# Kernel tuning notes

Measured on AMD Instinct MI355X. Metric: run time of the kernel, lower is better.

The kernel has to match this reference:

```python
import jax, jax.numpy as jnp
import numpy as np

B, QT, N, E, H = 4, 1024, 2048, 512, 8
Dh = E // H
ROPE_BASE = 10000.0


def rope_cos_sin_from_pos(pos_idx, Dh, base=10000.0, dtype=jnp.float32):
    # pos_idx: [B, T] -> cos, sin: [B, T, Dh]
    half = Dh // 2
    freqs = 1.0 / base ** (jnp.arange(0, half, dtype=dtype) / half)
    ang = pos_idx.astype(dtype)[..., None] * freqs[None, None, :]
    cos = jnp.repeat(jnp.cos(ang), 2, axis=-1)
    sin = jnp.repeat(jnp.sin(ang), 2, axis=-1)
    return cos, sin


def rope_apply(x_hd, cos, sin):
    # x_hd: [B, H, T, Dh]; cos/sin: [B, 1, T, Dh] (only first Dh//2 used, as in source)
    D = x_hd.shape[-1]
    x2 = x_hd.reshape(*x_hd.shape[:-1], D // 2, 2)
    x1, xi = x2[..., 0], x2[..., 1]
    c = cos[..., :D // 2]
    s = sin[..., :D // 2]
    y1 = x1 * c - xi * s
    y2 = x1 * s + xi * c
    return jnp.stack([y1, y2], axis=-1).reshape(*x_hd.shape)


def setup_inputs() -> dict:
    key = jax.random.key(0)
    ks = jax.random.split(key, 16)
    scale_w = 1.0 / np.sqrt(E)
    inp = {
        "q": jax.random.normal(ks[0], (B, QT, E), jnp.float32),
        "kv": jax.random.normal(ks[1], (B, N, E), jnp.float32),
        "q_mask": jax.random.randint(ks[2], (B, QT), 0, 2) > 0,
        "kv_mask": jax.random.randint(ks[3], (B, N), 0, 2) > 0,
        "q_pos_idx": jnp.sort(jax.random.randint(ks[4], (B, QT), 0, 4096), axis=-1).astype(jnp.int32),
        "kv_pos_idx": jnp.sort(jax.random.randint(ks[5], (B, N), 0, 4096), axis=-1).astype(jnp.int32),
        "Wq": jax.random.normal(ks[6], (E, E), jnp.float32) * scale_w,
        "bq": jnp.zeros((E,), jnp.float32),
        "Wk": jax.random.normal(ks[7], (E, E), jnp.float32) * scale_w,
        "bk": jnp.zeros((E,), jnp.float32),
        "Wv": jax.random.normal(ks[8], (E, E), jnp.float32) * scale_w,
        "bv": jnp.zeros((E,), jnp.float32),
        "Wo": jax.random.normal(ks[9], (E, E), jnp.float32) * scale_w,
        "bo": jnp.zeros((E,), jnp.float32),
    }
    return inp


def reference(q, kv, q_mask, kv_mask, q_pos_idx, kv_pos_idx,
              Wq, bq, Wk, bk, Wv, bv, Wo, bo):
    scale = 1.0 / jnp.sqrt(jnp.array(Dh, dtype=q.dtype))
    # projections -> [B, H, T, Dh]
    qh = (q @ Wq + bq).reshape(B, QT, H, Dh).transpose(0, 2, 1, 3)
    kh = (kv @ Wk + bk).reshape(B, N, H, Dh).transpose(0, 2, 1, 3)
    vh = (kv @ Wv + bv).reshape(B, N, H, Dh).transpose(0, 2, 1, 3)
    # per-sample RoPE
    cos_q, sin_q = rope_cos_sin_from_pos(q_pos_idx, Dh, ROPE_BASE, qh.dtype)
    cos_k, sin_k = rope_cos_sin_from_pos(kv_pos_idx, Dh, ROPE_BASE, kh.dtype)
    qh = rope_apply(qh, cos_q[:, None], sin_q[:, None])
    kh = rope_apply(kh, cos_k[:, None], sin_k[:, None])
    # scores [B, H, Q, N]
    scores = jnp.einsum("bhqd,bhkd->bhqk", qh, kh) * scale
    kvm = kv_mask[:, None, None, :].astype(bool)
    scores = jnp.where(kvm, scores, jnp.full_like(scores, -1e9))
    attn = jax.nn.softmax(scores, axis=-1)
    # dropout_rate=0 / deterministic -> identity; post-softmax mask + renorm
    attn = attn * kvm
    attn = attn / (attn.sum(-1, keepdims=True) + 1e-9)
    ctx = jnp.einsum("bhqk,bhkd->bhqd", attn, vh)
    ctx = ctx.transpose(0, 2, 1, 3).reshape(B, QT, E)
    ctx = ctx @ Wo + bo
    ctx = ctx * q_mask.astype(ctx.dtype)[:, :, None]
    return ctx, attn
```

## Files before the change

kernel.cpp:

```cpp
#include <hip/hip_runtime.h>
#include <hip/hip_bf16.h>

#define B_  4
#define QT_ 1024
#define N_  2048
#define E_  512
#define H_  8
#define DH_ 64

typedef float  f32x4  __attribute__((ext_vector_type(4)));
typedef __bf16 bf16x8 __attribute__((ext_vector_type(8)));
typedef unsigned short u16;
typedef u16 u16x4 __attribute__((ext_vector_type(4)));

static __device__ __forceinline__ u16 f2bf(float f) {
    unsigned u = __builtin_bit_cast(unsigned, f);
    return (u16)((u + 0x7fffu + ((u >> 16) & 1u)) >> 16);
}

static __device__ __forceinline__ bf16x8 ldbf8(const u16* p) {
    uint4 v = *reinterpret_cast<const uint4*>(p);
    return __builtin_bit_cast(bf16x8, v);
}

#define MFMA16(a, b, c) __builtin_amdgcn_mfma_f32_16x16x32_bf16((a), (b), (c), 0, 0, 0)

static __device__ __forceinline__ void g2lds16(const u16* g, u16* l) {
    __builtin_amdgcn_global_load_lds((__attribute__((address_space(1))) void*)(void*)g,
                                     (__attribute__((address_space(3))) void*)l, 16, 0, 0);
}

__global__ __launch_bounds__(256) void cvt_all(const float* __restrict__ q,
                                               const float* __restrict__ kv,
                                               u16* __restrict__ qbf,
                                               u16* __restrict__ kvbf) {
    const int QN4 = B_ * QT_ * E_ / 4;
    int i = blockIdx.x * 256 + threadIdx.x;
    const float4* s;
    ushort4* d;
    if (i < QN4) {
        s = reinterpret_cast<const float4*>(q) + i;
        d = reinterpret_cast<ushort4*>(qbf) + i;
    } else {
        int j = i - QN4;
        s = reinterpret_cast<const float4*>(kv) + j;
        d = reinterpret_cast<ushort4*>(kvbf) + j;
    }
    float4 v = *s;
    ushort4 o;
    o.x = f2bf(v.x); o.y = f2bf(v.y); o.z = f2bf(v.z); o.w = f2bf(v.w);
    *d = o;
}

__global__ __launch_bounds__(256) void wt_all(const float* __restrict__ Wq,
                                              const float* __restrict__ Wk,
                                              const float* __restrict__ Wv,
                                              const float* __restrict__ Wo,
                                              u16* __restrict__ wt4) {
    __shared__ float t[64][65];
    const float* W = (blockIdx.z == 0) ? Wq : (blockIdx.z == 1) ? Wk : (blockIdx.z == 2) ? Wv : Wo;
    u16* dst = wt4 + (size_t)blockIdx.z * E_ * E_;
    int k0 = blockIdx.x * 64, n0 = blockIdx.y * 64;
    int tid = threadIdx.x;
#pragma unroll
    for (int i = 0; i < 16; i++) {
        int idx = tid + i * 256, r = idx >> 6, c = idx & 63;
        t[r][c] = W[(k0 + r) * E_ + n0 + c];
    }
    __syncthreads();
#pragma unroll
    for (int i = 0; i < 16; i++) {
        int idx = tid + i * 256, r = idx >> 6, c = idx & 63;
        dst[(n0 + r) * E_ + k0 + c] = f2bf(t[c][r]);
    }
}

__global__ __launch_bounds__(256) void rope_all(const int* __restrict__ qpos,
                                                const int* __restrict__ kvpos,
                                                float2* __restrict__ tq,
                                                float2* __restrict__ tk) {
    const int QROWS = B_ * QT_;
    int i = blockIdx.x * 256 + threadIdx.x;
    int k = i & 15, row = i >> 4;
    float fr = exp2f((float)k * -0.41524101186092028f);
    int p;
    float2* dst;
    if (row < QROWS) { p = qpos[row]; dst = tq + i; }
    else { p = kvpos[row - QROWS]; dst = tk + (i - QROWS * 16); }
    float sn, cs;
    sincosf((float)p * fr, &sn, &cs);
    *dst = make_float2(cs, sn);
}

__global__ __launch_bounds__(256) void proj_qkv(const u16* __restrict__ qbf,
                                                const u16* __restrict__ kvbf,
                                                const u16* __restrict__ wt4,
                                                const float* __restrict__ bq,
                                                const float* __restrict__ bk,
                                                const float* __restrict__ bv,
                                                u16* __restrict__ qhh,
                                                u16* __restrict__ khh,
                                                u16* __restrict__ vt,
                                                const float2* __restrict__ tq,
                                                const float2* __restrict__ tk) {
    __shared__ __align__(16) u16 la[2][128 * 32];
    __shared__ __align__(16) u16 lb[2][128 * 32];

    const int id = blockIdx.x;
    const int sw = (id & 7) * 80 + (id >> 3);
    const bool isQ = (sw < 128);
    int m0, n0;
    const u16 *X, *W;
    if (isQ) { m0 = (sw >> 2) * 128; n0 = (sw & 3) * 128; X = qbf; W = wt4; }
    else { const int s2 = sw - 128; m0 = (s2 >> 3) * 128; n0 = (s2 & 7) * 128; X = kvbf; W = wt4 + 512 * 512; }

    const int tid = threadIdx.x, w = tid >> 6, lane = tid & 63;
    const int lr = lane & 15, lg = lane >> 4;
    const int wml = (w >> 1) * 64, wnl = (w & 1) * 64;

    auto stage = [&](const u16* gsrc, u16* lbuf) {
#pragma unroll
        for (int i = 0; i < 2; i++) {
            const int r0 = w * 32 + i * 16;
            const int row = r0 + (lane >> 2);
            const u16* src = gsrc + row * E_ + (((lane & 3) ^ (row & 3)) * 8);
            g2lds16(src, lbuf + r0 * 32);
        }
    };

    f32x4 acc[4][4];
#pragma unroll
    for (int i = 0; i < 4; i++)
#pragma unroll
        for (int j = 0; j < 4; j++) acc[i][j] = f32x4{0.f, 0.f, 0.f, 0.f};

    stage(X + m0 * E_, la[0]);
    stage(W + n0 * E_, lb[0]);
    __syncthreads();
    int buf = 0;
    for (int kt = 0; kt < E_ / 32; kt++) {
        if (kt + 1 < E_ / 32) {
            stage(X + m0 * E_ + (kt + 1) * 32, la[buf ^ 1]);
            stage(W + n0 * E_ + (kt + 1) * 32, lb[buf ^ 1]);
        }
        bf16x8 a[4], bb[4];
#pragma unroll
        for (int mb = 0; mb < 4; mb++) {
            const int r = wml + mb * 16 + lr;
            a[mb] = ldbf8(la[buf] + r * 32 + ((lg ^ (r & 3)) * 8));
        }
#pragma unroll
        for (int nb = 0; nb < 4; nb++) {
            const int r = wnl + nb * 16 + lr;
            bb[nb] = ldbf8(lb[buf] + r * 32 + ((lg ^ (r & 3)) * 8));
        }
        __builtin_amdgcn_s_setprio(1);
#pragma unroll
        for (int mb = 0; mb < 4; mb++)
#pragma unroll
            for (int nb = 0; nb < 4; nb++)
                acc[mb][nb] = MFMA16(a[mb], bb[nb], acc[mb][nb]);
        __builtin_amdgcn_s_setprio(0);
        __syncthreads();
        buf ^= 1;
    }

    const bool isV = !isQ && (n0 >= 512);
#pragma unroll
    for (int mb = 0; mb < 4; mb++) {
#pragma unroll
        for (int nb = 0; nb < 4; nb++) {
            const int col = n0 + wnl + nb * 16 + lr;
            const float bs = isQ ? bq[col] : (isV ? bv[col - 512] : bk[col]);
#pragma unroll
            for (int r = 0; r < 4; r++) {
                const int row = m0 + wml + mb * 16 + lg * 4 + r;
                float v = acc[mb][nb][r] + bs;
                if (isV) {
                    const int cv = col - 512, d = cv & 63, h = cv >> 6;
                    const int b = row >> 11, n = row & 2047;
                    vt[(((b * H_ + h) * (N_ / 64) + (n >> 6)) * DH_ + d) * 64 + (n & 63)] = f2bf(v);
                } else {
                    const int d = col & 63, h = col >> 6;
                    float2 t = isQ ? tq[row * 16 + (d >> 2)] : tk[row * 16 + (d >> 2)];
                    float other = __shfl_xor(v, 1);
                    float y = (d & 1) ? (other * t.y + v * t.x) : (v * t.x - other * t.y);
                    if (isQ) {
                        y *= 0.125f;
                        const int b = row >> 10, tok = row & 1023;
                        qhh[((b * H_ + h) * QT_ + tok) * DH_ + d] = f2bf(y);
                    } else {
                        const int b = row >> 11, tok = row & 2047;
                        khh[((b * H_ + h) * N_ + tok) * DH_ + d] = f2bf(y);
                    }
                }
            }
        }
    }
}

__global__ __launch_bounds__(256) void attn_sums(const u16* __restrict__ qh,
                                                 const u16* __restrict__ kh,
                                                 const int* __restrict__ kv_mask,
                                                 float* __restrict__ sums4) {
    __shared__ __align__(16) u16 kbuf[2][64 * 64];

    const int id = blockIdx.x;
    const int sw = (id & 7) * 256 + (id >> 3);
    const int bh = sw >> 6, qt = (sw >> 2) & 15, ns = sw & 3;
    const int b = bh >> 3;
    const int tid = threadIdx.x, w = tid >> 6, lane = tid & 63;
    const int lr = lane & 15, lg = lane >> 4;
    const int q0 = qt * 64 + w * 16;

    const u16* qbase = qh + (bh * QT_ + q0) * DH_;
    const bf16x8 qf0 = ldbf8(qbase + lr * DH_ + lg * 8);
    const bf16x8 qf1 = ldbf8(qbase + lr * DH_ + 32 + lg * 8);
    const u16* kbase = kh + (size_t)bh * (N_ * DH_) + ns * 512 * DH_;
    const int* mbase = kv_mask + b * N_ + ns * 512;

    auto stage = [&](const u16* gsrc, u16* lbuf) {
#pragma unroll
        for (int i = 0; i < 2; i++) {
            const int r0 = w * 16 + i * 8;
            const int row = r0 + (lane >> 3);
            const u16* src = gsrc + row * 64 + (((lane & 7) ^ (row & 7)) * 8);
            g2lds16(src, lbuf + r0 * 64);
        }
    };

    float lsum[4] = {0.f, 0.f, 0.f, 0.f};
    stage(kbase, kbuf[0]);
    __syncthreads();
    for (int t = 0; t < 8; t++) {
        const u16* kc = kbuf[t & 1];
        if (t < 7) stage(kbase + (t + 1) * (64 * DH_), kbuf[(t + 1) & 1]);
#pragma unroll
        for (int n = 0; n < 4; n++) {
            const int krow = n * 16 + lr;
            const u16* kp = kc + krow * 64;
            bf16x8 k0 = ldbf8(kp + ((lg ^ (krow & 7)) * 8));
            bf16x8 k1 = ldbf8(kp + (((lg + 4) ^ (krow & 7)) * 8));
            f32x4 c = f32x4{0.f, 0.f, 0.f, 0.f};
            __builtin_amdgcn_s_setprio(1);
            c = MFMA16(qf0, k0, c);
            c = MFMA16(qf1, k1, c);
            __builtin_amdgcn_s_setprio(0);
            const bool keep = (mbase[t * 64 + n * 16 + lr] != 0);
#pragma unroll
            for (int r = 0; r < 4; r++) lsum[r] += keep ? __expf(c[r]) : 0.f;
        }
        __syncthreads();
    }
#pragma unroll
    for (int r = 0; r < 4; r++) {
        float s = lsum[r];
        s += __shfl_xor(s, 1); s += __shfl_xor(s, 2);
        s += __shfl_xor(s, 4); s += __shfl_xor(s, 8);
        if (lr == 0) sums4[((size_t)bh * QT_ + q0 + lg * 4 + r) * 4 + ns] = s;
    }
}

__global__ __launch_bounds__(256) void attn_pv(const u16* __restrict__ qh,
                                               const u16* __restrict__ kh,
                                               const u16* __restrict__ vt,
                                               const int* __restrict__ kv_mask,
                                               const float* __restrict__ sums4,
                                               float* __restrict__ attn_out,
                                               float* __restrict__ pvpart) {
    __shared__ __align__(16) u16 kbuf[2][64 * 64];
    __shared__ __align__(16) u16 vbuf[2][64 * 64];
    __shared__ unsigned PW[4][16][32];

    const int id = blockIdx.x;
    const int sw = (id & 7) * 128 + (id >> 3);
    const int bh = sw >> 5, qt = (sw >> 1) & 15, ns = sw & 1;
    const int b = bh >> 3;
    const int tid = threadIdx.x, w = tid >> 6, lane = tid & 63;
    const int lr = lane & 15, lg = lane >> 4;
    const int q0 = qt * 64 + w * 16;

    const u16* qbase = qh + (bh * QT_ + q0) * DH_;
    const bf16x8 qf0 = ldbf8(qbase + lr * DH_ + lg * 8);
    const bf16x8 qf1 = ldbf8(qbase + lr * DH_ + 32 + lg * 8);
    const u16* kbase = kh + (size_t)bh * (N_ * DH_) + ns * 1024 * DH_;
    const u16* vbase = vt + (size_t)bh * (N_ * DH_) + ns * 1024 * DH_;
    const int* mbase = kv_mask + b * N_ + ns * 1024;

    float inv[4];
#pragma unroll
    for (int r = 0; r < 4; r++) {
        float4 s4 = *reinterpret_cast<const float4*>(
            sums4 + ((size_t)bh * QT_ + q0 + lg * 4 + r) * 4);
        float tot = s4.x + s4.y + s4.z + s4.w;
        inv[r] = (tot > 0.f) ? (1.0f / tot) : 0.f;
    }

    auto stage = [&](const u16* gsrc, u16* lbuf) {
#pragma unroll
        for (int i = 0; i < 2; i++) {
            const int r0 = w * 16 + i * 8;
            const int row = r0 + (lane >> 3);
            const u16* src = gsrc + row * 64 + (((lane & 7) ^ (row & 7)) * 8);
            g2lds16(src, lbuf + r0 * 64);
        }
    };

    f32x4 pv[4];
#pragma unroll
    for (int i = 0; i < 4; i++) pv[i] = f32x4{0.f, 0.f, 0.f, 0.f};
    unsigned(*P)[32] = PW[w];
    float* abase = attn_out + ((size_t)(bh * QT_ + q0)) * N_ + ns * 1024;
    const int srow = lane >> 4, cq = lane & 15;

    stage(kbase, kbuf[0]);
    stage(vbase, vbuf[0]);
    __syncthreads();
    for (int t = 0; t < 16; t++) {
        const u16* kc = kbuf[t & 1];
        const u16* vc = vbuf[t & 1];
        if (t < 15) {
            stage(kbase + (t + 1) * (64 * DH_), kbuf[(t + 1) & 1]);
            stage(vbase + (t + 1) * (64 * DH_), vbuf[(t + 1) & 1]);
        }
#pragma unroll
        for (int n = 0; n < 4; n++) {
            const int krow = n * 16 + lr;
            const u16* kp = kc + krow * 64;
            bf16x8 k0 = ldbf8(kp + ((lg ^ (krow & 7)) * 8));
            bf16x8 k1 = ldbf8(kp + (((lg + 4) ^ (krow & 7)) * 8));
            f32x4 c = f32x4{0.f, 0.f, 0.f, 0.f};
            __builtin_amdgcn_s_setprio(1);
            c = MFMA16(qf0, k0, c);
            c = MFMA16(qf1, k1, c);
            __builtin_amdgcn_s_setprio(0);
            const bool keep = (mbase[t * 64 + n * 16 + lr] != 0);
#pragma unroll
            for (int r = 0; r < 4; r++) {
                float p = keep ? (__expf(c[r]) * inv[r]) : 0.f;
                float hi = __shfl_xor(p, 1);
                __bf16 lo_b = (__bf16)p, hi_b = (__bf16)hi;
                unsigned pk = ((unsigned)__builtin_bit_cast(u16, hi_b) << 16) |
                              (unsigned)__builtin_bit_cast(u16, lo_b);
                if (!(lr & 1)) {
                    const int row = lg * 4 + r, c32 = n * 8 + (lr >> 1);
                    P[row][(((c32 >> 2) ^ (row & 7)) << 2) + (c32 & 3)] = pk;
                }
            }
        }
#pragma unroll
        for (int i = 0; i < 4; i++) {
            const int row = i * 4 + srow, rw = row & 7;
            const int m = (((cq >> 1) ^ rw) << 2) + ((cq & 1) << 1);
            uint2 pp = *reinterpret_cast<const uint2*>(&P[row][m]);
            f32x4 vv;
            vv[0] = __builtin_bit_cast(float, pp.x << 16);
            vv[1] = __builtin_bit_cast(float, pp.x & 0xffff0000u);
            vv[2] = __builtin_bit_cast(float, pp.y << 16);
            vv[3] = __builtin_bit_cast(float, pp.y & 0xffff0000u);
            *reinterpret_cast<f32x4*>(abase + (size_t)row * N_ + t * 64 + cq * 4) = vv;
        }
#pragma unroll
        for (int ks = 0; ks < 2; ks++) {
            const int g = (4 * ks + lg) ^ (lr & 7);
            uint4 a4 = *reinterpret_cast<const uint4*>(&P[lr][g << 2]);
            bf16x8 af = __builtin_bit_cast(bf16x8, a4);
            __builtin_amdgcn_s_setprio(1);
#pragma unroll
            for (int nb = 0; nb < 4; nb++) {
                const int vrow = nb * 16 + lr;
                bf16x8 bv = ldbf8(vc + vrow * 64 + (((ks * 4 + lg) ^ (vrow & 7)) * 8));
                pv[nb] = MFMA16(af, bv, pv[nb]);
            }
            __builtin_amdgcn_s_setprio(0);
        }
        __syncthreads();
    }

    float* pbase = pvpart + (((size_t)ns * 32 + bh) * QT_) * DH_;
#pragma unroll
    for (int nb = 0; nb < 4; nb++)
#pragma unroll
        for (int r = 0; r < 4; r++)
            pbase[(size_t)(q0 + lg * 4 + r) * DH_ + nb * 16 + lr] = pv[nb][r];
}

__global__ __launch_bounds__(256) void ctx_reduce(const float* __restrict__ pvpart,
                                                  u16* __restrict__ ctx) {
    const int i = blockIdx.x * 256 + threadIdx.x;
    const int base = i * 4;
    const int d = base & 63, h = (base >> 6) & 7;
    const int bt = base >> 9;
    const size_t pi = (((size_t)(bt >> 10) * 8 + h) * QT_ + (bt & 1023)) * DH_ + d;
    f32x4 s0 = *reinterpret_cast<const f32x4*>(pvpart + pi);
    f32x4 s1 = *reinterpret_cast<const f32x4*>(pvpart + (size_t)32 * QT_ * DH_ + pi);
    u16x4 o;
#pragma unroll
    for (int j = 0; j < 4; j++) o[j] = f2bf(s0[j] + s1[j]);
    *reinterpret_cast<u16x4*>(ctx + base) = o;
}

__global__ __launch_bounds__(256) void proj_o(const u16* __restrict__ X,
                                              const u16* __restrict__ Wt,
                                              const float* __restrict__ bias,
                                              float* __restrict__ outp,
                                              const int* __restrict__ qmask) {
    __shared__ __align__(16) u16 la[2][64 * 64];
    __shared__ __align__(16) u16 lb[2][64 * 64];

    const int id = blockIdx.x;
    const int sw = (id & 7) * 64 + (id >> 3);
    const int m0 = (sw >> 3) * 64, n0 = (sw & 7) * 64;

    const int tid = threadIdx.x, w = tid >> 6, lane = tid & 63;
    const int lr = lane & 15, lg = lane >> 4;
    const int wml = (w >> 1) * 32, wnl = (w & 1) * 32;

    auto stage = [&](const u16* gsrc, u16* lbuf) {
#pragma unroll
        for (int i = 0; i < 2; i++) {
            const int r0 = w * 16 + i * 8;
            const int row = r0 + (lane >> 3);
            const u16* src = gsrc + row * E_ + (((lane & 7) ^ (row & 7)) * 8);
            g2lds16(src, lbuf + r0 * 64);
        }
    };

    f32x4 acc[2][2];
#pragma unroll
    for (int i = 0; i < 2; i++)
#pragma unroll
        for (int j = 0; j < 2; j++) acc[i][j] = f32x4{0.f, 0.f, 0.f, 0.f};

    stage(X + m0 * E_, la[0]);
    stage(Wt + n0 * E_, lb[0]);
    __syncthreads();
    int buf = 0;
    for (int kt = 0; kt < E_ / 64; kt++) {
        if (kt + 1 < E_ / 64) {
            stage(X + m0 * E_ + (kt + 1) * 64, la[buf ^ 1]);
            stage(Wt + n0 * E_ + (kt + 1) * 64, lb[buf ^ 1]);
        }
#pragma unroll
        for (int ks = 0; ks < 2; ks++) {
            bf16x8 a[2], bb[2];
#pragma unroll
            for (int mb = 0; mb < 2; mb++) {
                const int r = wml + mb * 16 + lr;
                a[mb] = ldbf8(la[buf] + r * 64 + (((ks * 4 + lg) ^ (r & 7)) * 8));
            }
#pragma unroll
            for (int nb = 0; nb < 2; nb++) {
                const int r = wnl + nb * 16 + lr;
                bb[nb] = ldbf8(lb[buf] + r * 64 + (((ks * 4 + lg) ^ (r & 7)) * 8));
            }
            __builtin_amdgcn_s_setprio(1);
#pragma unroll
            for (int mb = 0; mb < 2; mb++)
#pragma unroll
                for (int nb = 0; nb < 2; nb++)
                    acc[mb][nb] = MFMA16(a[mb], bb[nb], acc[mb][nb]);
            __builtin_amdgcn_s_setprio(0);
        }
        __syncthreads();
        buf ^= 1;
    }

#pragma unroll
    for (int mb = 0; mb < 2; mb++) {
#pragma unroll
        for (int nb = 0; nb < 2; nb++) {
            const int col = n0 + wnl + nb * 16 + lr;
            const float bs = bias[col];
#pragma unroll
            for (int r = 0; r < 4; r++) {
                const int row = m0 + wml + mb * 16 + lg * 4 + r;
                float v = acc[mb][nb][r] + bs;
                float m = (qmask[row] != 0) ? 1.0f : 0.0f;
                outp[row * E_ + col] = v * m;
            }
        }
    }
}

extern "C" void kernel_launch(void* const* d_in, const int* in_sizes, int n_in,
                              void* d_out, int out_size, void* d_ws, size_t ws_size,
                              hipStream_t stream) {
    (void)in_sizes; (void)n_in; (void)out_size; (void)ws_size;
    const float* q   = (const float*)d_in[0];
    const float* kv  = (const float*)d_in[1];
    const int* q_mask  = (const int*)d_in[2];
    const int* kv_mask = (const int*)d_in[3];
    const int* q_pos   = (const int*)d_in[4];
    const int* kv_pos  = (const int*)d_in[5];
    const float* Wq = (const float*)d_in[6];  const float* bq = (const float*)d_in[7];
    const float* Wk = (const float*)d_in[8];  const float* bk = (const float*)d_in[9];
    const float* Wv = (const float*)d_in[10]; const float* bv = (const float*)d_in[11];
    const float* Wo = (const float*)d_in[12]; const float* bo = (const float*)d_in[13];
    float* outp = (float*)d_out;

    char* ws = (char*)d_ws;
    size_t off = 0;
    auto carve = [&](size_t bytes) -> void* {
        void* p = ws + off;
        off = (off + bytes + 255) & ~(size_t)255;
        return p;
    };
    u16* qbf    = (u16*)carve((size_t)B_ * QT_ * E_ * 2);
    u16* kvbf   = (u16*)carve((size_t)B_ * N_ * E_ * 2);
    u16* wt4    = (u16*)carve((size_t)4 * E_ * E_ * 2);
    u16* qhh    = (u16*)carve((size_t)B_ * H_ * QT_ * DH_ * 2);
    u16* khh    = (u16*)carve((size_t)B_ * H_ * N_ * DH_ * 2);
    u16* vt     = (u16*)carve((size_t)B_ * H_ * DH_ * N_ * 2);
    u16* ctx    = (u16*)carve((size_t)B_ * QT_ * E_ * 2);
    float2* tq  = (float2*)carve((size_t)B_ * QT_ * 16 * sizeof(float2));
    float2* tk  = (float2*)carve((size_t)B_ * N_ * 16 * sizeof(float2));
    float* sums4  = (float*)carve((size_t)B_ * H_ * QT_ * 4 * sizeof(float));
    float* pvpart = (float*)carve((size_t)2 * B_ * H_ * QT_ * DH_ * sizeof(float));

    cvt_all<<<6144, 256, 0, stream>>>(q, kv, qbf, kvbf);
    wt_all<<<dim3(8, 8, 4), 256, 0, stream>>>(Wq, Wk, Wv, Wo, wt4);
    rope_all<<<768, 256, 0, stream>>>(q_pos, kv_pos, tq, tk);

    proj_qkv<<<640, 256, 0, stream>>>(qbf, kvbf, wt4, bq, bk, bv, qhh, khh, vt, tq, tk);

    attn_sums<<<2048, 256, 0, stream>>>(qhh, khh, kv_mask, sums4);
    attn_pv<<<1024, 256, 0, stream>>>(qhh, khh, vt, kv_mask, sums4,
                                      outp + (size_t)B_ * QT_ * E_, pvpart);
    ctx_reduce<<<2048, 256, 0, stream>>>(pvpart, ctx);

    proj_o<<<512, 256, 0, stream>>>(ctx, wt4 + 3 * 512 * 512, bo, outp, q_mask);
}
```

Baseline: 161.7 us.

## Drop LDS staging in attention kernels, split PV over four key chunks

Both attention kernels now read K and V fragments straight from global memory (relying on cache) instead of double-buffering them through LDS with barriers, and they get launch-bound occupancy hints. attn_pv's key split grows from two to four chunks, doubling its grid, and ctx_reduce now sums four partial buffers. This removes barrier and LDS traffic and raises parallelism, but adds redundant global and L2 reads across waves and a larger partial-sum buffer to write and reduce.

```diff
diff --git a/kernel.cpp b/kernel.cpp
--- a/kernel.cpp
+++ b/kernel.cpp
@@ -199,12 +199,10 @@
     }
 }
 
-__global__ __launch_bounds__(256) void attn_sums(const u16* __restrict__ qh,
-                                                 const u16* __restrict__ kh,
-                                                 const int* __restrict__ kv_mask,
-                                                 float* __restrict__ sums4) {
-    __shared__ __align__(16) u16 kbuf[2][64 * 64];
-
+__global__ __launch_bounds__(256, 8) void attn_sums(const u16* __restrict__ qh,
+                                                    const u16* __restrict__ kh,
+                                                    const int* __restrict__ kv_mask,
+                                                    float* __restrict__ sums4) {
     const int id = blockIdx.x;
     const int sw = (id & 7) * 256 + (id >> 3);
     const int bh = sw >> 6, qt = (sw >> 2) & 15, ns = sw & 3;
@@ -219,122 +217,81 @@
     const u16* kbase = kh + (size_t)bh * (N_ * DH_) + ns * 512 * DH_;
     const int* mbase = kv_mask + b * N_ + ns * 512;
 
-    auto stage = [&](const u16* gsrc, u16* lbuf) {
-#pragma unroll
-        for (int i = 0; i < 2; i++) {
-            const int r0 = w * 16 + i * 8;
-            const int row = r0 + (lane >> 3);
-            const u16* src = gsrc + row * 64 + (((lane & 7) ^ (row & 7)) * 8);
-            g2lds16(src, lbuf + r0 * 64);
-        }
-    };
-
     float lsum[4] = {0.f, 0.f, 0.f, 0.f};
-    stage(kbase, kbuf[0]);
-    __syncthreads();
+    for (int kb = 0; kb < 32; kb++) {
+        const int krow = kb * 16 + lr;
+        bf16x8 k0 = ldbf8(kbase + krow * DH_ + lg * 8);
+        bf16x8 k1 = ldbf8(kbase + krow * DH_ + 32 + lg * 8);
+        f32x4 c = f32x4{0.f, 0.f, 0.f, 0.f};
+        __builtin_amdgcn_s_setprio(1);
+        c = MFMA16(qf0, k0, c);
+        c = MFMA16(qf1, k1, c);
+        __builtin_amdgcn_s_setprio(0);
+        const bool keep = (mbase[krow] != 0);
+#pragma unroll
+        for (int r = 0; r < 4; r++) lsum[r] += keep ? __expf(c[r]) : 0.f;
+    }
+#pragma unroll
+    for (int r = 0; r < 4; r++) {
+        float s = lsum[r];
+        s += __shfl_xor(s, 1); s += __shfl_xor(s, 2);
+        s += __shfl_xor(s, 4); s += __shfl_xor(s, 8);
+        if (lr == 0) sums4[((size_t)bh * QT_ + q0 + lg * 4 + r) * 4 + ns] = s;
+    }
+}
+
+__global__ __launch_bounds__(256, 6) void attn_pv(const u16* __restrict__ qh,
+                                                  const u16* __restrict__ kh,
+                                                  const u16* __restrict__ vt,
+                                                  const int* __restrict__ kv_mask,
+                                                  const float* __restrict__ sums4,
+                                                  float* __restrict__ attn_out,
+                                                  float* __restrict__ pvpart) {
+    __shared__ unsigned PW[4][16][32];
+
+    const int id = blockIdx.x;
+    const int sw = (id & 7) * 256 + (id >> 3);
+    const int bh = sw >> 6, qt = (sw >> 2) & 15, ns = sw & 3;
+    const int b = bh >> 3;
+    const int tid = threadIdx.x, w = tid >> 6, lane = tid & 63;
+    const int lr = lane & 15, lg = lane >> 4;
+    const int q0 = qt * 64 + w * 16;
+
+    const u16* qbase = qh + (bh * QT_ + q0) * DH_;
+    const bf16x8 qf0 = ldbf8(qbase + lr * DH_ + lg * 8);
+    const bf16x8 qf1 = ldbf8(qbase + lr * DH_ + 32 + lg * 8);
+    const u16* kbase = kh + (size_t)bh * (N_ * DH_) + ns * 512 * DH_;
+    const u16* vbase = vt + (size_t)bh * (N_ * DH_) + ns * 512 * DH_;
+    const int* mbase = kv_mask + b * N_ + ns * 512;
+
+    float inv[4];
+#pragma unroll
+    for (int r = 0; r < 4; r++) {
+        float4 s4 = *reinterpret_cast<const float4*>(
+            sums4 + ((size_t)bh * QT_ + q0 + lg * 4 + r) * 4);
+        float tot = s4.x + s4.y + s4.z + s4.w;
+        inv[r] = (tot > 0.f) ? (1.0f / tot) : 0.f;
+    }
+
+    f32x4 pv[4];
+#pragma unroll
+    for (int i = 0; i < 4; i++) pv[i] = f32x4{0.f, 0.f, 0.f, 0.f};
+    unsigned(*P)[32] = PW[w];
+    float* abase = attn_out + ((size_t)(bh * QT_ + q0)) * N_ + ns * 512;
+    const int srow = lane >> 4, cq = lane & 15;
+
     for (int t = 0; t < 8; t++) {
-        const u16* kc = kbuf[t & 1];
-        if (t < 7) stage(kbase + (t + 1) * (64 * DH_), kbuf[(t + 1) & 1]);
 #pragma unroll
         for (int n = 0; n < 4; n++) {
-            const int krow = n * 16 + lr;
-            const u16* kp = kc + krow * 64;
-            bf16x8 k0 = ldbf8(kp + ((lg ^ (krow & 7)) * 8));
-            bf16x8 k1 = ldbf8(kp + (((lg + 4) ^ (krow & 7)) * 8));
+            const int krow = t * 64 + n * 16 + lr;
+            bf16x8 k0 = ldbf8(kbase + krow * DH_ + lg * 8);
+            bf16x8 k1 = ldbf8(kbase + krow * DH_ + 32 + lg * 8);
             f32x4 c = f32x4{0.f, 0.f, 0.f, 0.f};
             __builtin_amdgcn_s_setprio(1);
             c = MFMA16(qf0, k0, c);
             c = MFMA16(qf1, k1, c);
             __builtin_amdgcn_s_setprio(0);
-            const bool keep = (mbase[t * 64 + n * 16 + lr] != 0);
-#pragma unroll
-            for (int r = 0; r < 4; r++) lsum[r] += keep ? __expf(c[r]) : 0.f;
-        }
-        __syncthreads();
-    }
-#pragma unroll
-    for (int r = 0; r < 4; r++) {
-        float s = lsum[r];
-        s += __shfl_xor(s, 1); s += __shfl_xor(s, 2);
-        s += __shfl_xor(s, 4); s += __shfl_xor(s, 8);
-        if (lr == 0) sums4[((size_t)bh * QT_ + q0 + lg * 4 + r) * 4 + ns] = s;
-    }
-}
-
-__global__ __launch_bounds__(256) void attn_pv(const u16* __restrict__ qh,
-                                               const u16* __restrict__ kh,
-                                               const u16* __restrict__ vt,
-                                               const int* __restrict__ kv_mask,
-                                               const float* __restrict__ sums4,
-                                               float* __restrict__ attn_out,
-                                               float* __restrict__ pvpart) {
-    __shared__ __align__(16) u16 kbuf[2][64 * 64];
-    __shared__ __align__(16) u16 vbuf[2][64 * 64];
-    __shared__ unsigned PW[4][16][32];
-
-    const int id = blockIdx.x;
-    const int sw = (id & 7) * 128 + (id >> 3);
-    const int bh = sw >> 5, qt = (sw >> 1) & 15, ns = sw & 1;
-    const int b = bh >> 3;
-    const int tid = threadIdx.x, w = tid >> 6, lane = tid & 63;
-    const int lr = lane & 15, lg = lane >> 4;
-    const int q0 = qt * 64 + w * 16;
-
-    const u16* qbase = qh + (bh * QT_ + q0) * DH_;
-    const bf16x8 qf0 = ldbf8(qbase + lr * DH_ + lg * 8);
-    const bf16x8 qf1 = ldbf8(qbase + lr * DH_ + 32 + lg * 8);
-    const u16* kbase = kh + (size_t)bh * (N_ * DH_) + ns * 1024 * DH_;
-    const u16* vbase = vt + (size_t)bh * (N_ * DH_) + ns * 1024 * DH_;
-    const int* mbase = kv_mask + b * N_ + ns * 1024;
-
-    float inv[4];
-#pragma unroll
-    for (int r = 0; r < 4; r++) {
-        float4 s4 = *reinterpret_cast<const float4*>(
-            sums4 + ((size_t)bh * QT_ + q0 + lg * 4 + r) * 4);
-        float tot = s4.x + s4.y + s4.z + s4.w;
-        inv[r] = (tot > 0.f) ? (1.0f / tot) : 0.f;
-    }
-
-    auto stage = [&](const u16* gsrc, u16* lbuf) {
-#pragma unroll
-        for (int i = 0; i < 2; i++) {
-            const int r0 = w * 16 + i * 8;
-            const int row = r0 + (lane >> 3);
-            const u16* src = gsrc + row * 64 + (((lane & 7) ^ (row & 7)) * 8);
-            g2lds16(src, lbuf + r0 * 64);
-        }
-    };
-
-    f32x4 pv[4];
-#pragma unroll
-    for (int i = 0; i < 4; i++) pv[i] = f32x4{0.f, 0.f, 0.f, 0.f};
-    unsigned(*P)[32] = PW[w];
-    float* abase = attn_out + ((size_t)(bh * QT_ + q0)) * N_ + ns * 1024;
-    const int srow = lane >> 4, cq = lane & 15;
-
-    stage(kbase, kbuf[0]);
-    stage(vbase, vbuf[0]);
-    __syncthreads();
-    for (int t = 0; t < 16; t++) {
-        const u16* kc = kbuf[t & 1];
-        const u16* vc = vbuf[t & 1];
-        if (t < 15) {
-            stage(kbase + (t + 1) * (64 * DH_), kbuf[(t + 1) & 1]);
-            stage(vbase + (t + 1) * (64 * DH_), vbuf[(t + 1) & 1]);
-        }
-#pragma unroll
-        for (int n = 0; n < 4; n++) {
-            const int krow = n * 16 + lr;
-            const u16* kp = kc + krow * 64;
-            bf16x8 k0 = ldbf8(kp + ((lg ^ (krow & 7)) * 8));
-            bf16x8 k1 = ldbf8(kp + (((lg + 4) ^ (krow & 7)) * 8));
-            f32x4 c = f32x4{0.f, 0.f, 0.f, 0.f};
-            __builtin_amdgcn_s_setprio(1);
-            c = MFMA16(qf0, k0, c);
-            c = MFMA16(qf1, k1, c);
-            __builtin_amdgcn_s_setprio(0);
-            const bool keep = (mbase[t * 64 + n * 16 + lr] != 0);
+            const bool keep = (mbase[krow] != 0);
 #pragma unroll
             for (int r = 0; r < 4; r++) {
                 float p = keep ? (__expf(c[r]) * inv[r]) : 0.f;
@@ -368,13 +325,12 @@
             __builtin_amdgcn_s_setprio(1);
 #pragma unroll
             for (int nb = 0; nb < 4; nb++) {
-                const int vrow = nb * 16 + lr;
-                bf16x8 bv = ldbf8(vc + vrow * 64 + (((ks * 4 + lg) ^ (vrow & 7)) * 8));
+                const int vrow = t * 64 + nb * 16 + lr;
+                bf16x8 bv = ldbf8(vbase + vrow * 64 + ks * 32 + lg * 8);
                 pv[nb] = MFMA16(af, bv, pv[nb]);
             }
             __builtin_amdgcn_s_setprio(0);
         }
-        __syncthreads();
     }
 
     float* pbase = pvpart + (((size_t)ns * 32 + bh) * QT_) * DH_;
@@ -387,16 +343,19 @@
 
 __global__ __launch_bounds__(256) void ctx_reduce(const float* __restrict__ pvpart,
                                                   u16* __restrict__ ctx) {
+    const size_t SL = (size_t)32 * QT_ * DH_;
     const int i = blockIdx.x * 256 + threadIdx.x;
     const int base = i * 4;
     const int d = base & 63, h = (base >> 6) & 7;
     const int bt = base >> 9;
     const size_t pi = (((size_t)(bt >> 10) * 8 + h) * QT_ + (bt & 1023)) * DH_ + d;
     f32x4 s0 = *reinterpret_cast<const f32x4*>(pvpart + pi);
-    f32x4 s1 = *reinterpret_cast<const f32x4*>(pvpart + (size_t)32 * QT_ * DH_ + pi);
+    f32x4 s1 = *reinterpret_cast<const f32x4*>(pvpart + SL + pi);
+    f32x4 s2 = *reinterpret_cast<const f32x4*>(pvpart + 2 * SL + pi);
+    f32x4 s3 = *reinterpret_cast<const f32x4*>(pvpart + 3 * SL + pi);
     u16x4 o;
 #pragma unroll
-    for (int j = 0; j < 4; j++) o[j] = f2bf(s0[j] + s1[j]);
+    for (int j = 0; j < 4; j++) o[j] = f2bf((s0[j] + s1[j]) + (s2[j] + s3[j]));
     *reinterpret_cast<u16x4*>(ctx + base) = o;
 }
 
@@ -516,7 +475,7 @@
     float2* tq  = (float2*)carve((size_t)B_ * QT_ * 16 * sizeof(float2));
     float2* tk  = (float2*)carve((size_t)B_ * N_ * 16 * sizeof(float2));
     float* sums4  = (float*)carve((size_t)B_ * H_ * QT_ * 4 * sizeof(float));
-    float* pvpart = (float*)carve((size_t)2 * B_ * H_ * QT_ * DH_ * sizeof(float));
+    float* pvpart = (float*)carve((size_t)4 * B_ * H_ * QT_ * DH_ * sizeof(float));
 
     cvt_all<<<6144, 256, 0, stream>>>(q, kv, qbf, kvbf);
     wt_all<<<dim3(8, 8, 4), 256, 0, stream>>>(Wq, Wk, Wv, Wo, wt4);
@@ -525,7 +484,7 @@
     proj_qkv<<<640, 256, 0, stream>>>(qbf, kvbf, wt4, bq, bk, bv, qhh, khh, vt, tq, tk);
 
     attn_sums<<<2048, 256, 0, stream>>>(qhh, khh, kv_mask, sums4);
-    attn_pv<<<1024, 256, 0, stream>>>(qhh, khh, vt, kv_mask, sums4,
+    attn_pv<<<2048, 256, 0, stream>>>(qhh, khh, vt, kv_mask, sums4,
                                       outp + (size_t)B_ * QT_ * E_, pvpart);
     ctx_reduce<<<2048, 256, 0, stream>>>(pvpart, ctx);
 
```

Measured after the change: 280.6 us. +73.5%, slower.
